# Optimization experiments

Measured on AMD Instinct MI355X. Metric: run time of the kernel, lower is better.

The kernel has to match this reference:

```python
import jax, jax.numpy as jnp
import numpy as np

E = 1024
H = 8
B = 32768
EPS = 1e-5


def setup_inputs() -> dict:
    key = jax.random.key(0)
    ks = jax.random.split(key, 12)
    s = 1.0 / np.sqrt(E)
    return {
        "user_emb": jax.random.normal(ks[0], (B, E), jnp.float32),
        "item_emb": jax.random.normal(ks[1], (B, E), jnp.float32),
        # user_to_item_attention params (torch MultiheadAttention layout)
        "u2i_in_w": jax.random.uniform(ks[2], (3 * E, E), jnp.float32, -s, s),
        "u2i_in_b": jnp.zeros((3 * E,), jnp.float32),
        "u2i_out_w": jax.random.uniform(ks[3], (E, E), jnp.float32, -s, s),
        "u2i_out_b": jnp.zeros((E,), jnp.float32),
        # item_to_user_attention params
        "i2u_in_w": jax.random.uniform(ks[4], (3 * E, E), jnp.float32, -s, s),
        "i2u_in_b": jnp.zeros((3 * E,), jnp.float32),
        "i2u_out_w": jax.random.uniform(ks[5], (E, E), jnp.float32, -s, s),
        "i2u_out_b": jnp.zeros((E,), jnp.float32),
        # LayerNorms
        "user_norm_g": jnp.ones((E,), jnp.float32),
        "user_norm_b": jnp.zeros((E,), jnp.float32),
        "item_norm_g": jnp.ones((E,), jnp.float32),
        "item_norm_b": jnp.zeros((E,), jnp.float32),
        # residual scales
        "alpha": jnp.full((1,), 0.1, jnp.float32),
        "beta": jnp.full((1,), 0.1, jnp.float32),
    }


def _mha_seq1(q_in, kv_in, in_w, in_b, out_w, out_b):
    # torch MHA with query seq_len=1 and key/value seq_len=1 (dropout in eval mode).
    d = E // H
    Wq, Wk, Wv = in_w[:E], in_w[E:2 * E], in_w[2 * E:]
    bq, bk, bv = in_b[:E], in_b[E:2 * E], in_b[2 * E:]
    q = (q_in @ Wq.T + bq).reshape(-1, H, d)   # [B,H,d]
    k = (kv_in @ Wk.T + bk).reshape(-1, H, d)
    v = (kv_in @ Wv.T + bv).reshape(-1, H, d)
    scores = jnp.sum(q * k, axis=-1, keepdims=True) / jnp.sqrt(jnp.float32(d))  # [B,H,1]
    w = jax.nn.softmax(scores, axis=-1)  # single key -> exactly 1
    attn = (w * v).reshape(-1, E)
    return attn @ out_w.T + out_b


def _layernorm(x, g, b):
    mu = jnp.mean(x, axis=-1, keepdims=True)
    var = jnp.mean(jnp.square(x - mu), axis=-1, keepdims=True)
    return (x - mu) * jax.lax.rsqrt(var + EPS) * g + b


def reference(user_emb, item_emb, u2i_in_w, u2i_in_b, u2i_out_w, u2i_out_b,
              i2u_in_w, i2u_in_b, i2u_out_w, i2u_out_b,
              user_norm_g, user_norm_b, item_norm_g, item_norm_b, alpha, beta):
    user_att = _mha_seq1(user_emb, item_emb, u2i_in_w, u2i_in_b, u2i_out_w, u2i_out_b)
    item_att = _mha_seq1(item_emb, user_emb, i2u_in_w, i2u_in_b, i2u_out_w, i2u_out_b)
    user_evolved = _layernorm(user_emb + alpha * user_att, user_norm_g, user_norm_b)
    item_evolved = _layernorm(item_emb + beta * item_att, item_norm_g, item_norm_b)
    return (user_evolved, item_evolved)
```

## Files before the change

kernel.cpp:

```cpp
#include <hip/hip_runtime.h>
#include <cstdint>
#include <cstddef>

#define E 1024
#define NB 32768
#define BM 128
#define BN 128

typedef __attribute__((ext_vector_type(4))) float f32x4;
typedef __attribute__((ext_vector_type(8))) short bf16x8;
typedef __attribute__((ext_vector_type(4))) short s16x4;

__device__ __forceinline__ short f2bfs(float x) {
    __bf16 h = (__bf16)x;
    return __builtin_bit_cast(short, h);
}
__device__ __forceinline__ float bf2f(short u) {
    union { unsigned u; float f; } v;
    v.u = ((unsigned)(unsigned short)u) << 16;
    return v.f;
}
__device__ __forceinline__ bf16x8 cvt8(f32x4 lo, f32x4 hi) {
    bf16x8 r;
#pragma unroll
    for (int j = 0; j < 4; ++j) { r[j] = f2bfs(lo[j]); r[j + 4] = f2bfs(hi[j]); }
    return r;
}

__device__ __forceinline__ void gload16(const void* g, void* l) {
    __builtin_amdgcn_global_load_lds(
        (__attribute__((address_space(1))) void*)g,
        (__attribute__((address_space(3))) void*)l, 16, 0, 0);
}

__global__ __launch_bounds__(256) void wv_transpose(const float* W0, short* T0,
                                                    const float* W1, short* T1) {
    const float* W = blockIdx.z ? W1 : W0;
    short* T = blockIdx.z ? T1 : T0;
    __shared__ float tile[32][33];
    const int j0 = blockIdx.x * 32, i0 = blockIdx.y * 32;
    const int tx = threadIdx.x, ty = threadIdx.y;
#pragma unroll
    for (int r = 0; r < 4; ++r)
        tile[ty + 8 * r][tx] = W[(size_t)(i0 + ty + 8 * r) * E + j0 + tx];
    __syncthreads();
#pragma unroll
    for (int r = 0; r < 4; ++r)
        T[(size_t)(j0 + ty + 8 * r) * E + i0 + tx] = f2bfs(tile[tx][ty + 8 * r]);
}

__global__ __launch_bounds__(256) void bias_fuse(const float* O0, const float* bv0, const float* ob0, const float* s0, float* c0,
                                                 const float* O1, const float* bv1, const float* ob1, const float* s1, float* c1) {
    const float* O  = blockIdx.z ? O1 : O0;
    const float* bv = blockIdx.z ? bv1 : bv0;
    const float* ob = blockIdx.z ? ob1 : ob0;
    const float* sc = blockIdx.z ? s1 : s0;
    float* c = blockIdx.z ? c1 : c0;
    const int n = blockIdx.x, t = threadIdx.x;
    float s = 0.f;
    for (int i = t; i < E; i += 256) s += O[(size_t)n * E + i] * bv[i];
#pragma unroll
    for (int o = 32; o; o >>= 1) s += __shfl_down(s, o);
    __shared__ float rs[4];
    if ((t & 63) == 0) rs[t >> 6] = s;
    __syncthreads();
    if (t == 0) c[n] = sc[0] * (rs[0] + rs[1] + rs[2] + rs[3] + ob[n]);
}

struct GemmArgs {
    const char* A;
    const short* B;
    const float* bias;
    const float* scale;
    char* C;
};

template <bool ABF16>
__global__ __launch_bounds__(256, ABF16 ? 4 : 3) void gemm_bt(GemmArgs g0, GemmArgs g1,
                                                              int mb, int arstride, int crstride) {
    const int nwg = gridDim.x;
    const int q = nwg >> 3;
    const int wgid = (blockIdx.x & 7) * q + (blockIdx.x >> 3);
    const int per = mb * 8;
    const int z = wgid / per;
    const int rem = wgid - z * per;
    const int bx = rem >> 3;
    const int by = rem & 7;
    GemmArgs ga = z ? g1 : g0;

    constexpr int ABYTES = ABF16 ? 8192 : 16384;
    constexpr int BUFB = ABYTES + 8192;
    __shared__ __align__(16) char lds[2][BUFB];

    const int t = threadIdx.x;
    const int l = t & 63, w = t >> 6;
    const int am0 = bx * BM, bn0 = by * BN;

    const char* gA[ABF16 ? 2 : 4];
    if constexpr (ABF16) {
#pragma unroll
        for (int i = 0; i < 2; ++i) {
            int c = i * 4 + w;
            int row = c * 16 + (l >> 2);
            int slot = (l & 3) ^ ((row >> 1) & 3);
            gA[i] = ga.A + (size_t)(am0 + row) * arstride + slot * 16;
        }
    } else {
#pragma unroll
        for (int i = 0; i < 4; ++i) {
            int c = i * 4 + w;
            int row = c * 8 + (l >> 3);
            int slot = (l & 7) ^ (row & 7);
            gA[i] = ga.A + (size_t)(am0 + row) * arstride + slot * 16;
        }
    }
    const short* gB[2];
#pragma unroll
    for (int i = 0; i < 2; ++i) {
        int c = i * 4 + w;
        int row = c * 16 + (l >> 2);
        int slot = (l & 3) ^ ((row >> 1) & 3);
        gB[i] = ga.B + (size_t)(bn0 + row) * E + slot * 8;
    }

    auto stage = [&](int buf, int kt) {
        if constexpr (ABF16) {
#pragma unroll
            for (int i = 0; i < 2; ++i)
                gload16(gA[i] + (size_t)kt * 2, &lds[buf][(i * 4 + w) * 1024]);
        } else {
#pragma unroll
            for (int i = 0; i < 4; ++i)
                gload16(gA[i] + (size_t)kt * 4, &lds[buf][(i * 4 + w) * 1024]);
        }
#pragma unroll
        for (int i = 0; i < 2; ++i)
            gload16(gB[i] + kt, &lds[buf][ABYTES + (i * 4 + w) * 1024]);
    };

    const int wm = w >> 1, wn = w & 1;
    const int r16 = l & 15, kg = l >> 4;
    int aoff[4][ABF16 ? 1 : 2], boff[4];
#pragma unroll
    for (int m = 0; m < 4; ++m) {
        int row = wm * 64 + m * 16 + r16;
        if constexpr (ABF16) {
            aoff[m][0] = row * 64 + (kg ^ ((row >> 1) & 3)) * 16;
        } else {
            aoff[m][0] = row * 128 + ((kg * 2) ^ (row & 7)) * 16;
            aoff[m][1] = row * 128 + ((kg * 2 + 1) ^ (row & 7)) * 16;
        }
    }
#pragma unroll
    for (int n = 0; n < 4; ++n) {
        int row = wn * 64 + n * 16 + r16;
        boff[n] = ABYTES + row * 64 + (kg ^ ((row >> 1) & 3)) * 16;
    }

    f32x4 acc[4][4] = {};

    auto compute = [&](int buf) {
        bf16x8 a[4], b[4];
#pragma unroll
        for (int m = 0; m < 4; ++m) {
            if constexpr (ABF16) {
                a[m] = *(const bf16x8*)&lds[buf][aoff[m][0]];
            } else {
                f32x4 lo = *(const f32x4*)&lds[buf][aoff[m][0]];
                f32x4 hi = *(const f32x4*)&lds[buf][aoff[m][1]];
                a[m] = cvt8(lo, hi);
            }
        }
#pragma unroll
        for (int n = 0; n < 4; ++n)
            b[n] = *(const bf16x8*)&lds[buf][boff[n]];
#pragma unroll
        for (int m = 0; m < 4; ++m)
#pragma unroll
            for (int n = 0; n < 4; ++n)
                acc[m][n] = __builtin_amdgcn_mfma_f32_16x16x32_bf16(a[m], b[n], acc[m][n], 0, 0, 0);
    };

    stage(0, 0);
    __syncthreads();
#pragma unroll 1
    for (int kt = 0; kt < E; kt += 64) {
        stage(1, kt + 32);
        compute(0);
        __syncthreads();
        if (kt + 64 < E) stage(0, kt + 64);
        compute(1);
        __syncthreads();
    }

    const int ccol0 = bn0 + wn * 64 + r16;
    const int crow0 = am0 + wm * 64 + kg * 4;
    const float sc = ga.scale ? ga.scale[0] : 1.f;
    float bn_[4];
#pragma unroll
    for (int n = 0; n < 4; ++n) bn_[n] = ga.bias ? ga.bias[ccol0 + n * 16] : 0.f;
#pragma unroll
    for (int m = 0; m < 4; ++m)
#pragma unroll
        for (int n = 0; n < 4; ++n)
#pragma unroll
            for (int qq = 0; qq < 4; ++qq) {
                int row = crow0 + m * 16 + qq;
                int col = ccol0 + n * 16;
                short* p = (short*)(ga.C + (size_t)row * crstride) + col;
                *p = f2bfs(acc[m][n][qq] * sc + bn_[n]);
            }
}

struct FArgs {
    const float* kv;
    const short* M;
    const float* c;
    const float* q;
    const float* g;
    const float* b;
    float* out;
};

__global__ __launch_bounds__(512, 2) void fused_gemm_ln(FArgs f0, FArgs f1) {
    const int bid = blockIdx.x;
    const int u = bid >> 3, xcd = bid & 7;
    const int z = u & 1;
    const int mb = xcd * 64 + (u >> 1);
    const FArgs fa = z ? f1 : f0;
    const int r0 = mb * 64;

    __shared__ __align__(16) char lds[147456];

    const int t = threadIdx.x;
    const int l = t & 63, w = t >> 6;
    const int r16 = l & 15, kg = l >> 4;

    int bsrc[8];
#pragma unroll
    for (int c = 0; c < 8; ++c) {
        int gi = c * 512 + t;
        int row = gi >> 2, slot = gi & 3;
        bsrc[c] = row * 2048 + (slot ^ ((row >> 1) & 3)) * 16;
    }
    const char* Abase = (const char*)fa.kv + (size_t)(r0 + (t >> 3)) * 4096
                        + ((t & 7) ^ ((t >> 3) & 7)) * 16;

    auto stageB = [&](int buf, int kt) {
#pragma unroll
        for (int c = 0; c < 8; ++c)
            gload16((const char*)fa.M + bsrc[c] + kt * 2,
                    &lds[16384 + buf * 65536 + c * 8192 + w * 1024]);
    };
    auto stageA = [&](int buf, int kt) {
        gload16(Abase + (size_t)kt * 4, &lds[buf * 8192 + w * 1024]);
    };

    int aoff0[4], aoff1[4], boff[8];
#pragma unroll
    for (int m = 0; m < 4; ++m) {
        int row = m * 16 + r16;
        aoff0[m] = row * 128 + ((kg * 2) ^ (row & 7)) * 16;
        aoff1[m] = row * 128 + ((kg * 2 + 1) ^ (row & 7)) * 16;
    }
#pragma unroll
    for (int n = 0; n < 8; ++n) {
        int row = w * 128 + n * 16 + r16;
        boff[n] = 16384 + row * 64 + (kg ^ ((row >> 1) & 3)) * 16;
    }

    f32x4 acc[4][8] = {};

    auto phase = [&](int buf, int p) {
        const int abase = buf * 8192;
        const int bbase = buf * 65536;
        bf16x8 a[4], b[8];
#pragma unroll
        for (int m = 0; m < 4; ++m) {
            f32x4 lo = *(const f32x4*)&lds[abase + aoff0[m]];
            f32x4 hi = *(const f32x4*)&lds[abase + aoff1[m]];
            a[m] = cvt8(lo, hi);
        }
#pragma unroll
        for (int n = 0; n < 8; ++n)
            b[n] = *(const bf16x8*)&lds[bbase + boff[n]];
        asm volatile("s_waitcnt lgkmcnt(0)" ::: "memory");
        __builtin_amdgcn_sched_barrier(0);
        __builtin_amdgcn_s_barrier();
        const bool more = (p + 2) < 32;
        if (more) {
            stageA(buf, (p + 2) * 32);
            stageB(buf, (p + 2) * 32);
        }
        __builtin_amdgcn_s_setprio(1);
#pragma unroll
        for (int m = 0; m < 4; ++m)
#pragma unroll
            for (int n = 0; n < 8; ++n)
                acc[m][n] = __builtin_amdgcn_mfma_f32_16x16x32_bf16(a[m], b[n], acc[m][n], 0, 0, 0);
        __builtin_amdgcn_s_setprio(0);
        if (more) asm volatile("s_waitcnt vmcnt(9)" ::: "memory");
        else      asm volatile("s_waitcnt vmcnt(0)" ::: "memory");
        __builtin_amdgcn_sched_barrier(0);
        __builtin_amdgcn_s_barrier();
    };

    stageA(0, 0);  stageB(0, 0);
    stageA(1, 32); stageB(1, 32);
    asm volatile("s_waitcnt vmcnt(9)" ::: "memory");
    __builtin_amdgcn_sched_barrier(0);
    __builtin_amdgcn_s_barrier();

#pragma unroll 1
    for (int p = 0; p < 32; p += 2) {
        phase(0, p);
        phase(1, p + 1);
    }
    __builtin_amdgcn_s_barrier();

    float* S  = (float*)lds;
    float* Q  = (float*)(lds + 2048);
    float* CB = (float*)(lds + 4096);

    const int colbase = w * 128 + r16;
    float cf[8];
#pragma unroll
    for (int n = 0; n < 8; ++n) cf[n] = fa.c[colbase + n * 16];

    float sum_[4][4] = {}, sq_[4][4] = {};
#pragma unroll
    for (int m = 0; m < 4; ++m) {
#pragma unroll
        for (int n = 0; n < 8; ++n) {
#pragma unroll
            for (int qq = 0; qq < 4; ++qq) {
                int lrow = m * 16 + kg * 4 + qq;
                float x = acc[m][n][qq] + cf[n] + fa.q[(size_t)(r0 + lrow) * E + colbase + n * 16];
                acc[m][n][qq] = x;
                sum_[m][qq] += x;
                sq_[m][qq] += x * x;
            }
        }
    }
#pragma unroll
    for (int m = 0; m < 4; ++m)
#pragma unroll
        for (int qq = 0; qq < 4; ++qq)
#pragma unroll
            for (int o = 1; o < 16; o <<= 1) {
                sum_[m][qq] += __shfl_xor(sum_[m][qq], o);
                sq_[m][qq] += __shfl_xor(sq_[m][qq], o);
            }
#pragma unroll
    for (int m = 0; m < 4; ++m)
#pragma unroll
        for (int qq = 0; qq < 4; ++qq)
            if (r16 == m * 4 + qq) {
                int lrow = m * 16 + kg * 4 + qq;
                S[lrow * 8 + w] = sum_[m][qq];
                Q[lrow * 8 + w] = sq_[m][qq];
            }
    __syncthreads();
    if (t < 64) {
        f32x4 s0 = *(const f32x4*)(S + t * 8);
        f32x4 s1 = *(const f32x4*)(S + t * 8 + 4);
        f32x4 q0 = *(const f32x4*)(Q + t * 8);
        f32x4 q1 = *(const f32x4*)(Q + t * 8 + 4);
        float ss = s0[0] + s0[1] + s0[2] + s0[3] + s1[0] + s1[1] + s1[2] + s1[3];
        float qs = q0[0] + q0[1] + q0[2] + q0[3] + q1[0] + q1[1] + q1[2] + q1[3];
        float mean = ss * (1.0f / E);
        float var = qs * (1.0f / E) - mean * mean;
        CB[t * 2] = mean;
        CB[t * 2 + 1] = rsqrtf(var + 1e-5f);
    }
    __syncthreads();

    float gf[8], bf_[8];
#pragma unroll
    for (int n = 0; n < 8; ++n) {
        gf[n] = fa.g[colbase + n * 16];
        bf_[n] = fa.b[colbase + n * 16];
    }
#pragma unroll
    for (int m = 0; m < 4; ++m)
#pragma unroll
        for (int qq = 0; qq < 4; ++qq) {
            int lrow = m * 16 + kg * 4 + qq;
            float mean = CB[lrow * 2], rstd = CB[lrow * 2 + 1];
            float* op = fa.out + (size_t)(r0 + lrow) * E + colbase;
#pragma unroll
            for (int n = 0; n < 8; ++n)
                op[n * 16] = (acc[m][n][qq] - mean) * rstd * gf[n] + bf_[n];
        }
}

extern "C" void kernel_launch(void* const* d_in, const int* in_sizes, int n_in,
                              void* d_out, int out_size, void* d_ws, size_t ws_size,
                              hipStream_t stream) {
    const float* user_emb = (const float*)d_in[0];
    const float* item_emb = (const float*)d_in[1];
    const float* u2i_in_w = (const float*)d_in[2];
    const float* u2i_in_b = (const float*)d_in[3];
    const float* u2i_out_w = (const float*)d_in[4];
    const float* u2i_out_b = (const float*)d_in[5];
    const float* i2u_in_w = (const float*)d_in[6];
    const float* i2u_in_b = (const float*)d_in[7];
    const float* i2u_out_w = (const float*)d_in[8];
    const float* i2u_out_b = (const float*)d_in[9];
    const float* user_g = (const float*)d_in[10];
    const float* user_b = (const float*)d_in[11];
    const float* item_g = (const float*)d_in[12];
    const float* item_b = (const float*)d_in[13];
    const float* alpha = (const float*)d_in[14];
    const float* beta = (const float*)d_in[15];

    float* out_u = (float*)d_out;
    float* out_i = out_u + (size_t)NB * E;

    short* WvT1 = (short*)d_ws;
    short* WvT2 = WvT1 + (size_t)E * E;
    short* M1 = WvT2 + (size_t)E * E;
    short* M2 = M1 + (size_t)E * E;
    float* c1 = (float*)(M2 + (size_t)E * E);
    float* c2 = c1 + E;

    const dim3 b256(256);

    wv_transpose<<<dim3(32, 32, 2), dim3(32, 8), 0, stream>>>(
        u2i_in_w + 2 * (size_t)E * E, WvT1, i2u_in_w + 2 * (size_t)E * E, WvT2);

    bias_fuse<<<dim3(E, 1, 2), b256, 0, stream>>>(
        u2i_out_w, u2i_in_b + 2 * E, u2i_out_b, alpha, c1,
        i2u_out_w, i2u_in_b + 2 * E, i2u_out_b, beta, c2);

    gemm_bt<false><<<dim3(8 * 8 * 2), b256, 0, stream>>>(
        GemmArgs{(const char*)u2i_out_w, WvT1, nullptr, alpha, (char*)M1},
        GemmArgs{(const char*)i2u_out_w, WvT2, nullptr, beta, (char*)M2},
        8, 4096, 2048);

    fused_gemm_ln<<<dim3(1024), dim3(512), 0, stream>>>(
        FArgs{item_emb, M1, c1, user_emb, user_g, user_b, out_u},
        FArgs{user_emb, M2, c2, item_emb, item_g, item_b, out_i});
}
```

Before: 356.2 us.

## Convert A tile to bf16 in registers before LDS write, prefetch two stages ahead

The A operand (fp32 activations) no longer goes global→LDS as fp32 through async loads. Each thread now loads it into registers two phases ahead, converts it to bf16, and writes it to LDS. This halves the A tile's LDS footprint and moves the per-phase fp32→bf16 conversion off the MFMA-feeding LDS read path. The cost is register pressure, manual vmcnt bookkeeping and extra LDS write traffic plus an lgkmcnt wait before each barrier.

```diff
diff --git a/kernel.cpp b/kernel.cpp
--- a/kernel.cpp
+++ b/kernel.cpp
@@ -230,7 +230,7 @@
     const FArgs fa = z ? f1 : f0;
     const int r0 = mb * 64;
 
-    __shared__ __align__(16) char lds[147456];
+    __shared__ __align__(16) char lds[139264];
 
     const int t = threadIdx.x;
     const int l = t & 63, w = t >> 6;
@@ -243,55 +243,55 @@
         int row = gi >> 2, slot = gi & 3;
         bsrc[c] = row * 2048 + (slot ^ ((row >> 1) & 3)) * 16;
     }
-    const char* Abase = (const char*)fa.kv + (size_t)(r0 + (t >> 3)) * 4096
-                        + ((t & 7) ^ ((t >> 3) & 7)) * 16;
+    const int ar = t >> 3, ach = t & 7;
+    const float* asrc = fa.kv + (size_t)(r0 + ar) * E + ach * 4;
+    const int awoff = ar * 64 + (((ach >> 1) ^ ((ar >> 1) & 3)) * 16) + (ach & 1) * 8;
+
+    int aoff[4], boff[8];
+#pragma unroll
+    for (int m = 0; m < 4; ++m) {
+        int row = m * 16 + r16;
+        aoff[m] = row * 64 + (kg ^ ((row >> 1) & 3)) * 16;
+    }
+#pragma unroll
+    for (int n = 0; n < 8; ++n) {
+        int row = w * 128 + n * 16 + r16;
+        boff[n] = 8192 + row * 64 + (kg ^ ((row >> 1) & 3)) * 16;
+    }
+
+    f32x4 acc[4][8] = {};
 
     auto stageB = [&](int buf, int kt) {
 #pragma unroll
         for (int c = 0; c < 8; ++c)
             gload16((const char*)fa.M + bsrc[c] + kt * 2,
-                    &lds[16384 + buf * 65536 + c * 8192 + w * 1024]);
+                    &lds[8192 + buf * 65536 + c * 8192 + w * 1024]);
     };
-    auto stageA = [&](int buf, int kt) {
-        gload16(Abase + (size_t)kt * 4, &lds[buf * 8192 + w * 1024]);
+    auto commitA = [&](int buf, f32x4 av) {
+        s16x4 v;
+#pragma unroll
+        for (int j = 0; j < 4; ++j) v[j] = f2bfs(av[j]);
+        *(s16x4*)&lds[buf * 4096 + awoff] = v;
     };
 
-    int aoff0[4], aoff1[4], boff[8];
-#pragma unroll
-    for (int m = 0; m < 4; ++m) {
-        int row = m * 16 + r16;
-        aoff0[m] = row * 128 + ((kg * 2) ^ (row & 7)) * 16;
-        aoff1[m] = row * 128 + ((kg * 2 + 1) ^ (row & 7)) * 16;
-    }
-#pragma unroll
-    for (int n = 0; n < 8; ++n) {
-        int row = w * 128 + n * 16 + r16;
-        boff[n] = 16384 + row * 64 + (kg ^ ((row >> 1) & 3)) * 16;
-    }
-
-    f32x4 acc[4][8] = {};
-
-    auto phase = [&](int buf, int p) {
-        const int abase = buf * 8192;
-        const int bbase = buf * 65536;
+    auto phase = [&](int buf, int p, f32x4& areg) {
         bf16x8 a[4], b[8];
 #pragma unroll
-        for (int m = 0; m < 4; ++m) {
-            f32x4 lo = *(const f32x4*)&lds[abase + aoff0[m]];
-            f32x4 hi = *(const f32x4*)&lds[abase + aoff1[m]];
-            a[m] = cvt8(lo, hi);
-        }
+        for (int m = 0; m < 4; ++m)
+            a[m] = *(const bf16x8*)&lds[buf * 4096 + aoff[m]];
 #pragma unroll
         for (int n = 0; n < 8; ++n)
-            b[n] = *(const bf16x8*)&lds[bbase + boff[n]];
+            b[n] = *(const bf16x8*)&lds[buf * 65536 + boff[n]];
         asm volatile("s_waitcnt lgkmcnt(0)" ::: "memory");
         __builtin_amdgcn_sched_barrier(0);
         __builtin_amdgcn_s_barrier();
-        const bool more = (p + 2) < 32;
-        if (more) {
-            stageA(buf, (p + 2) * 32);
+        __builtin_amdgcn_sched_barrier(0);
+        if (p + 2 < 32) {
             stageB(buf, (p + 2) * 32);
-        }
+            commitA(buf, areg);
+        }
+        if (p + 4 < 32)
+            areg = *(const f32x4*)(asrc + (p + 4) * 32);
         __builtin_amdgcn_s_setprio(1);
 #pragma unroll
         for (int m = 0; m < 4; ++m)
@@ -299,24 +299,32 @@
             for (int n = 0; n < 8; ++n)
                 acc[m][n] = __builtin_amdgcn_mfma_f32_16x16x32_bf16(a[m], b[n], acc[m][n], 0, 0, 0);
         __builtin_amdgcn_s_setprio(0);
-        if (more) asm volatile("s_waitcnt vmcnt(9)" ::: "memory");
-        else      asm volatile("s_waitcnt vmcnt(0)" ::: "memory");
+        if (p <= 27)      asm volatile("s_waitcnt vmcnt(9)" ::: "memory");
+        else if (p <= 29) asm volatile("s_waitcnt vmcnt(8)" ::: "memory");
+        else              asm volatile("s_waitcnt vmcnt(0)" ::: "memory");
+        asm volatile("s_waitcnt lgkmcnt(0)" ::: "memory");
         __builtin_amdgcn_sched_barrier(0);
         __builtin_amdgcn_s_barrier();
     };
 
-    stageA(0, 0);  stageB(0, 0);
-    stageA(1, 32); stageB(1, 32);
-    asm volatile("s_waitcnt vmcnt(9)" ::: "memory");
+    f32x4 aE = *(const f32x4*)(asrc);
+    f32x4 aO = *(const f32x4*)(asrc + 32);
+    stageB(0, 0);
+    stageB(1, 32);
+    commitA(0, aE);
+    commitA(1, aO);
+    aE = *(const f32x4*)(asrc + 64);
+    aO = *(const f32x4*)(asrc + 96);
+    asm volatile("s_waitcnt vmcnt(10)" ::: "memory");
+    asm volatile("s_waitcnt lgkmcnt(0)" ::: "memory");
     __builtin_amdgcn_sched_barrier(0);
     __builtin_amdgcn_s_barrier();
 
 #pragma unroll 1
     for (int p = 0; p < 32; p += 2) {
-        phase(0, p);
-        phase(1, p + 1);
-    }
-    __builtin_amdgcn_s_barrier();
+        phase(0, p, aE);
+        phase(1, p + 1, aO);
+    }
 
     float* S  = (float*)lds;
     float* Q  = (float*)(lds + 2048);
```

After: 349.9 us. About the same (-1.8%).

## Restructure fused GEMM+LayerNorm to 1024 threads with register-staged bf16 A and LDS-staged residual

Applied to the files above, without the earlier changes.

The fused GEMM+LayerNorm kernel now runs 1024 threads per block, each wave covering 64 output columns. The B matrix (M) is read straight from global memory into registers instead of through LDS. Activation rows are loaded as float pairs into registers, converted to bf16 and written to a small double-buffered LDS tile. The residual q row block is prefetched during the K loop into LDS as bf16, which avoids a separate global read in the epilogue but rounds the residual to bf16. Alongside this, the unused ABF16 template path and bias handling are removed from gemm_bt.

```diff
diff --git a/kernel.cpp b/kernel.cpp
--- a/kernel.cpp
+++ b/kernel.cpp
@@ -8,8 +8,8 @@
 #define BN 128
 
 typedef __attribute__((ext_vector_type(4))) float f32x4;
+typedef __attribute__((ext_vector_type(2))) float f32x2;
 typedef __attribute__((ext_vector_type(8))) short bf16x8;
-typedef __attribute__((ext_vector_type(4))) short s16x4;
 
 __device__ __forceinline__ short f2bfs(float x) {
     __bf16 h = (__bf16)x;
@@ -25,6 +25,11 @@
 #pragma unroll
     for (int j = 0; j < 4; ++j) { r[j] = f2bfs(lo[j]); r[j + 4] = f2bfs(hi[j]); }
     return r;
+}
+__device__ __forceinline__ int pack2(f32x2 v) {
+    unsigned lo = (unsigned short)f2bfs(v[0]);
+    unsigned hi = (unsigned short)f2bfs(v[1]);
+    return (int)(lo | (hi << 16));
 }
 
 __device__ __forceinline__ void gload16(const void* g, void* l) {
@@ -75,9 +80,8 @@
     char* C;
 };
 
-template <bool ABF16>
-__global__ __launch_bounds__(256, ABF16 ? 4 : 3) void gemm_bt(GemmArgs g0, GemmArgs g1,
-                                                              int mb, int arstride, int crstride) {
+__global__ __launch_bounds__(256, 3) void gemm_bt(GemmArgs g0, GemmArgs g1,
+                                                  int mb, int arstride, int crstride) {
     const int nwg = gridDim.x;
     const int q = nwg >> 3;
     const int wgid = (blockIdx.x & 7) * q + (blockIdx.x >> 3);
@@ -88,7 +92,7 @@
     const int by = rem & 7;
     GemmArgs ga = z ? g1 : g0;
 
-    constexpr int ABYTES = ABF16 ? 8192 : 16384;
+    constexpr int ABYTES = 16384;
     constexpr int BUFB = ABYTES + 8192;
     __shared__ __align__(16) char lds[2][BUFB];
 
@@ -96,23 +100,13 @@
     const int l = t & 63, w = t >> 6;
     const int am0 = bx * BM, bn0 = by * BN;
 
-    const char* gA[ABF16 ? 2 : 4];
-    if constexpr (ABF16) {
-#pragma unroll
-        for (int i = 0; i < 2; ++i) {
-            int c = i * 4 + w;
-            int row = c * 16 + (l >> 2);
-            int slot = (l & 3) ^ ((row >> 1) & 3);
-            gA[i] = ga.A + (size_t)(am0 + row) * arstride + slot * 16;
-        }
-    } else {
-#pragma unroll
-        for (int i = 0; i < 4; ++i) {
-            int c = i * 4 + w;
-            int row = c * 8 + (l >> 3);
-            int slot = (l & 7) ^ (row & 7);
-            gA[i] = ga.A + (size_t)(am0 + row) * arstride + slot * 16;
-        }
+    const char* gA[4];
+#pragma unroll
+    for (int i = 0; i < 4; ++i) {
+        int c = i * 4 + w;
+        int row = c * 8 + (l >> 3);
+        int slot = (l & 7) ^ (row & 7);
+        gA[i] = ga.A + (size_t)(am0 + row) * arstride + slot * 16;
     }
     const short* gB[2];
 #pragma unroll
@@ -124,15 +118,9 @@
     }
 
     auto stage = [&](int buf, int kt) {
-        if constexpr (ABF16) {
-#pragma unroll
-            for (int i = 0; i < 2; ++i)
-                gload16(gA[i] + (size_t)kt * 2, &lds[buf][(i * 4 + w) * 1024]);
-        } else {
-#pragma unroll
-            for (int i = 0; i < 4; ++i)
-                gload16(gA[i] + (size_t)kt * 4, &lds[buf][(i * 4 + w) * 1024]);
-        }
+#pragma unroll
+        for (int i = 0; i < 4; ++i)
+            gload16(gA[i] + (size_t)kt * 4, &lds[buf][(i * 4 + w) * 1024]);
 #pragma unroll
         for (int i = 0; i < 2; ++i)
             gload16(gB[i] + kt, &lds[buf][ABYTES + (i * 4 + w) * 1024]);
@@ -140,16 +128,12 @@
 
     const int wm = w >> 1, wn = w & 1;
     const int r16 = l & 15, kg = l >> 4;
-    int aoff[4][ABF16 ? 1 : 2], boff[4];
+    int aoff[4][2], boff[4];
 #pragma unroll
     for (int m = 0; m < 4; ++m) {
         int row = wm * 64 + m * 16 + r16;
-        if constexpr (ABF16) {
-            aoff[m][0] = row * 64 + (kg ^ ((row >> 1) & 3)) * 16;
-        } else {
-            aoff[m][0] = row * 128 + ((kg * 2) ^ (row & 7)) * 16;
-            aoff[m][1] = row * 128 + ((kg * 2 + 1) ^ (row & 7)) * 16;
-        }
+        aoff[m][0] = row * 128 + ((kg * 2) ^ (row & 7)) * 16;
+        aoff[m][1] = row * 128 + ((kg * 2 + 1) ^ (row & 7)) * 16;
     }
 #pragma unroll
     for (int n = 0; n < 4; ++n) {
@@ -163,13 +147,9 @@
         bf16x8 a[4], b[4];
 #pragma unroll
         for (int m = 0; m < 4; ++m) {
-            if constexpr (ABF16) {
-                a[m] = *(const bf16x8*)&lds[buf][aoff[m][0]];
-            } else {
-                f32x4 lo = *(const f32x4*)&lds[buf][aoff[m][0]];
-                f32x4 hi = *(const f32x4*)&lds[buf][aoff[m][1]];
-                a[m] = cvt8(lo, hi);
-            }
+            f32x4 lo = *(const f32x4*)&lds[buf][aoff[m][0]];
+            f32x4 hi = *(const f32x4*)&lds[buf][aoff[m][1]];
+            a[m] = cvt8(lo, hi);
         }
 #pragma unroll
         for (int n = 0; n < 4; ++n)
@@ -196,9 +176,6 @@
     const int ccol0 = bn0 + wn * 64 + r16;
     const int crow0 = am0 + wm * 64 + kg * 4;
     const float sc = ga.scale ? ga.scale[0] : 1.f;
-    float bn_[4];
-#pragma unroll
-    for (int n = 0; n < 4; ++n) bn_[n] = ga.bias ? ga.bias[ccol0 + n * 16] : 0.f;
 #pragma unroll
     for (int m = 0; m < 4; ++m)
 #pragma unroll
@@ -208,7 +185,7 @@
                 int row = crow0 + m * 16 + qq;
                 int col = ccol0 + n * 16;
                 short* p = (short*)(ga.C + (size_t)row * crstride) + col;
-                *p = f2bfs(acc[m][n][qq] * sc + bn_[n]);
+                *p = f2bfs(acc[m][n][qq] * sc);
             }
 }
 
@@ -222,7 +199,12 @@
     float* out;
 };
 
-__global__ __launch_bounds__(512, 2) void fused_gemm_ln(FArgs f0, FArgs f1) {
+#define QLDS 8192
+#define SLDS 139264
+#define QLDS2 143360
+#define CBLDS 147456
+
+__global__ __launch_bounds__(1024) void fused_gemm_ln(FArgs f0, FArgs f1) {
     const int bid = blockIdx.x;
     const int u = bid >> 3, xcd = bid & 7;
     const int z = u & 1;
@@ -230,113 +212,105 @@
     const FArgs fa = z ? f1 : f0;
     const int r0 = mb * 64;
 
-    __shared__ __align__(16) char lds[147456];
+    __shared__ __align__(16) char lds[147968];
 
     const int t = threadIdx.x;
     const int l = t & 63, w = t >> 6;
     const int r16 = l & 15, kg = l >> 4;
 
-    int bsrc[8];
-#pragma unroll
-    for (int c = 0; c < 8; ++c) {
-        int gi = c * 512 + t;
-        int row = gi >> 2, slot = gi & 3;
-        bsrc[c] = row * 2048 + (slot ^ ((row >> 1) & 3)) * 16;
-    }
-    const char* Abase = (const char*)fa.kv + (size_t)(r0 + (t >> 3)) * 4096
-                        + ((t & 7) ^ ((t >> 3) & 7)) * 16;
-
-    auto stageB = [&](int buf, int kt) {
-#pragma unroll
-        for (int c = 0; c < 8; ++c)
-            gload16((const char*)fa.M + bsrc[c] + kt * 2,
-                    &lds[16384 + buf * 65536 + c * 8192 + w * 1024]);
+    const int ard = kg * 1024 + r16 * 16;
+    const int tr = t >> 4, kp = t & 15;
+    const float* Ag = fa.kv + (size_t)(r0 + tr) * E + kp * 2;
+    const float* Qg = fa.q + (size_t)(r0 + tr) * E + kp * 2;
+    const int awr = ((kp >> 2) << 10) + tr * 16 + (kp & 3) * 4;
+    const int qwr = QLDS + tr * 2048 + kp * 4;
+
+    const short* Mb = fa.M;
+    int boff[4];
+#pragma unroll
+    for (int nf = 0; nf < 4; ++nf)
+        boff[nf] = (w * 64 + nf * 16 + r16) * E + kg * 8;
+
+    f32x4 acc[4][4] = {};
+
+    auto wrA = [&](int buf, f32x2 v) {
+        *(int*)&lds[buf * 4096 + awr] = pack2(v);
     };
-    auto stageA = [&](int buf, int kt) {
-        gload16(Abase + (size_t)kt * 4, &lds[buf * 8192 + w * 1024]);
+    auto wrQ = [&](int p, f32x2 v) {
+        *(int*)&lds[qwr + p * 64] = pack2(v);
     };
 
-    int aoff0[4], aoff1[4], boff[8];
-#pragma unroll
-    for (int m = 0; m < 4; ++m) {
-        int row = m * 16 + r16;
-        aoff0[m] = row * 128 + ((kg * 2) ^ (row & 7)) * 16;
-        aoff1[m] = row * 128 + ((kg * 2 + 1) ^ (row & 7)) * 16;
-    }
-#pragma unroll
-    for (int n = 0; n < 8; ++n) {
-        int row = w * 128 + n * 16 + r16;
-        boff[n] = 16384 + row * 64 + (kg ^ ((row >> 1) & 3)) * 16;
-    }
-
-    f32x4 acc[4][8] = {};
-
-    auto phase = [&](int buf, int p) {
-        const int abase = buf * 8192;
-        const int bbase = buf * 65536;
-        bf16x8 a[4], b[8];
-#pragma unroll
-        for (int m = 0; m < 4; ++m) {
-            f32x4 lo = *(const f32x4*)&lds[abase + aoff0[m]];
-            f32x4 hi = *(const f32x4*)&lds[abase + aoff1[m]];
-            a[m] = cvt8(lo, hi);
-        }
-#pragma unroll
-        for (int n = 0; n < 8; ++n)
-            b[n] = *(const bf16x8*)&lds[bbase + boff[n]];
+    {
+        f32x2 a0 = *(const f32x2*)(Ag);
+        f32x2 a1 = *(const f32x2*)(Ag + 32);
+        wrA(0, a0);
+        wrA(1, a1);
+    }
+    f32x2 aE = *(const f32x2*)(Ag + 64);
+    f32x2 aO = *(const f32x2*)(Ag + 96);
+    f32x2 qE = *(const f32x2*)(Qg);
+    f32x2 qO = *(const f32x2*)(Qg + 32);
+    asm volatile("s_waitcnt lgkmcnt(0)" ::: "memory");
+    __builtin_amdgcn_sched_barrier(0);
+    __builtin_amdgcn_s_barrier();
+    __builtin_amdgcn_sched_barrier(0);
+
+    auto phase = [&](int buf, int p, f32x2& aq, f32x2& qq) {
+        bf16x8 a[4], b[4];
+#pragma unroll
+        for (int nf = 0; nf < 4; ++nf)
+            b[nf] = *(const bf16x8*)(Mb + boff[nf] + p * 32);
+#pragma unroll
+        for (int m = 0; m < 4; ++m)
+            a[m] = *(const bf16x8*)&lds[buf * 4096 + ard + m * 256];
         asm volatile("s_waitcnt lgkmcnt(0)" ::: "memory");
         __builtin_amdgcn_sched_barrier(0);
         __builtin_amdgcn_s_barrier();
-        const bool more = (p + 2) < 32;
-        if (more) {
-            stageA(buf, (p + 2) * 32);
-            stageB(buf, (p + 2) * 32);
-        }
+        __builtin_amdgcn_sched_barrier(0);
+        if (p + 2 < 32) wrA(buf, aq);
+        wrQ(p, qq);
+        if (p + 4 < 32) aq = *(const f32x2*)(Ag + (p + 4) * 32);
+        if (p + 2 < 32) qq = *(const f32x2*)(Qg + (p + 2) * 32);
         __builtin_amdgcn_s_setprio(1);
 #pragma unroll
         for (int m = 0; m < 4; ++m)
 #pragma unroll
-            for (int n = 0; n < 8; ++n)
-                acc[m][n] = __builtin_amdgcn_mfma_f32_16x16x32_bf16(a[m], b[n], acc[m][n], 0, 0, 0);
+            for (int nf = 0; nf < 4; ++nf)
+                acc[m][nf] = __builtin_amdgcn_mfma_f32_16x16x32_bf16(a[m], b[nf], acc[m][nf], 0, 0, 0);
         __builtin_amdgcn_s_setprio(0);
-        if (more) asm volatile("s_waitcnt vmcnt(9)" ::: "memory");
-        else      asm volatile("s_waitcnt vmcnt(0)" ::: "memory");
-        __builtin_amdgcn_sched_barrier(0);
-        __builtin_amdgcn_s_barrier();
     };
-
-    stageA(0, 0);  stageB(0, 0);
-    stageA(1, 32); stageB(1, 32);
-    asm volatile("s_waitcnt vmcnt(9)" ::: "memory");
-    __builtin_amdgcn_sched_barrier(0);
-    __builtin_amdgcn_s_barrier();
 
 #pragma unroll 1
     for (int p = 0; p < 32; p += 2) {
-        phase(0, p);
-        phase(1, p + 1);
-    }
-    __builtin_amdgcn_s_barrier();
-
-    float* S  = (float*)lds;
-    float* Q  = (float*)(lds + 2048);
-    float* CB = (float*)(lds + 4096);
-
-    const int colbase = w * 128 + r16;
-    float cf[8];
-#pragma unroll
-    for (int n = 0; n < 8; ++n) cf[n] = fa.c[colbase + n * 16];
+        phase(0, p, aE, qE);
+        phase(1, p + 1, aO, qO);
+    }
+    __syncthreads();
+
+    float* S  = (float*)(lds + SLDS);
+    float* Q  = (float*)(lds + QLDS2);
+    float* CB = (float*)(lds + CBLDS);
+
+    const int colbase = w * 64 + r16;
+    float cf[4], gf[4], bf_[4];
+#pragma unroll
+    for (int nf = 0; nf < 4; ++nf) {
+        cf[nf] = fa.c[colbase + nf * 16];
+        gf[nf] = fa.g[colbase + nf * 16];
+        bf_[nf] = fa.b[colbase + nf * 16];
+    }
 
     float sum_[4][4] = {}, sq_[4][4] = {};
 #pragma unroll
     for (int m = 0; m < 4; ++m) {
 #pragma unroll
-        for (int n = 0; n < 8; ++n) {
+        for (int nf = 0; nf < 4; ++nf) {
 #pragma unroll
             for (int qq = 0; qq < 4; ++qq) {
                 int lrow = m * 16 + kg * 4 + qq;
-                float x = acc[m][n][qq] + cf[n] + fa.q[(size_t)(r0 + lrow) * E + colbase + n * 16];
-                acc[m][n][qq] = x;
+                short qv = *(const short*)&lds[QLDS + lrow * 2048 + (colbase + nf * 16) * 2];
+                float x = acc[m][nf][qq] + cf[nf] + bf2f(qv);
+                acc[m][nf][qq] = x;
                 sum_[m][qq] += x;
                 sq_[m][qq] += x * x;
             }
@@ -357,17 +331,14 @@
         for (int qq = 0; qq < 4; ++qq)
             if (r16 == m * 4 + qq) {
                 int lrow = m * 16 + kg * 4 + qq;
-                S[lrow * 8 + w] = sum_[m][qq];
-                Q[lrow * 8 + w] = sq_[m][qq];
+                S[lrow * 16 + w] = sum_[m][qq];
+                Q[lrow * 16 + w] = sq_[m][qq];
             }
     __syncthreads();
     if (t < 64) {
-        f32x4 s0 = *(const f32x4*)(S + t * 8);
-        f32x4 s1 = *(const f32x4*)(S + t * 8 + 4);
-        f32x4 q0 = *(const f32x4*)(Q + t * 8);
-        f32x4 q1 = *(const f32x4*)(Q + t * 8 + 4);
-        float ss = s0[0] + s0[1] + s0[2] + s0[3] + s1[0] + s1[1] + s1[2] + s1[3];
-        float qs = q0[0] + q0[1] + q0[2] + q0[3] + q1[0] + q1[1] + q1[2] + q1[3];
+        float ss = 0.f, qs = 0.f;
+#pragma unroll
+        for (int i = 0; i < 16; ++i) { ss += S[t * 16 + i]; qs += Q[t * 16 + i]; }
         float mean = ss * (1.0f / E);
         float var = qs * (1.0f / E) - mean * mean;
         CB[t * 2] = mean;
@@ -375,12 +346,6 @@
     }
     __syncthreads();
 
-    float gf[8], bf_[8];
-#pragma unroll
-    for (int n = 0; n < 8; ++n) {
-        gf[n] = fa.g[colbase + n * 16];
-        bf_[n] = fa.b[colbase + n * 16];
-    }
 #pragma unroll
     for (int m = 0; m < 4; ++m)
 #pragma unroll
@@ -389,8 +354,8 @@
             float mean = CB[lrow * 2], rstd = CB[lrow * 2 + 1];
             float* op = fa.out + (size_t)(r0 + lrow) * E + colbase;
 #pragma unroll
-            for (int n = 0; n < 8; ++n)
-                op[n * 16] = (acc[m][n][qq] - mean) * rstd * gf[n] + bf_[n];
+            for (int nf = 0; nf < 4; ++nf)
+                op[nf * 16] = (acc[m][nf][qq] - mean) * rstd * gf[nf] + bf_[nf];
         }
 }
 
@@ -433,12 +398,12 @@
         u2i_out_w, u2i_in_b + 2 * E, u2i_out_b, alpha, c1,
         i2u_out_w, i2u_in_b + 2 * E, i2u_out_b, beta, c2);
 
-    gemm_bt<false><<<dim3(8 * 8 * 2), b256, 0, stream>>>(
+    gemm_bt<<<dim3(8 * 8 * 2), b256, 0, stream>>>(
         GemmArgs{(const char*)u2i_out_w, WvT1, nullptr, alpha, (char*)M1},
         GemmArgs{(const char*)i2u_out_w, WvT2, nullptr, beta, (char*)M2},
         8, 4096, 2048);
 
-    fused_gemm_ln<<<dim3(1024), dim3(512), 0, stream>>>(
+    fused_gemm_ln<<<dim3(1024), dim3(1024), 0, stream>>>(
         FArgs{item_emb, M1, c1, user_emb, user_g, user_b, out_u},
         FArgs{user_emb, M2, c2, item_emb, item_g, item_b, out_i});
 }
```

Result: slower. 527.2 us (+48.0%).
